# Optimization experiments

Hardware: AMD Instinct MI355X
Metric: run time of the kernel (lower is better)

Reference implementation:

```python
import math
import jax
import jax.numpy as jnp
import numpy as np

N_FFT = 2048
HOP = 512
WIN = 2048
N_FREQ = N_FFT // 2 + 1


def _make_buffers():
    # ISTFT synthesis kernel: inverse DFT basis with one-sided spectrum weights.
    n = np.arange(N_FFT, dtype=np.float32)
    k = np.arange(N_FREQ, dtype=np.float32)
    angles = 2.0 * np.pi * k[:, None] * n[None, :] / N_FFT
    w = np.full(N_FREQ, 2.0 / N_FFT, dtype=np.float32)
    w[0] = 1.0 / N_FFT
    if N_FFT % 2 == 0:
        w[-1] = 1.0 / N_FFT
    real_k = np.cos(angles) * w[:, None]
    imag_k = -np.sin(angles) * w[:, None]
    kernel = np.concatenate([real_k, imag_k], axis=0).astype(np.float32)  # [2*N_FREQ, N_FFT]
    # periodic Hann window (torch.hann_window default), win_length == n_fft so no pad
    win = (0.5 * (1.0 - np.cos(2.0 * np.pi * np.arange(WIN) / WIN))).astype(np.float32)
    window_sq = (win * win).astype(np.float32)
    return jnp.asarray(kernel), jnp.asarray(window_sq)


def setup_inputs() -> dict:
    key = jax.random.key(0)
    B, frames = 8, 2048
    stft_repr = jax.random.normal(key, (B, N_FREQ, frames, 2), dtype=jnp.float32)
    kernel, window_sq = _make_buffers()
    orig_len = (frames - 1) * HOP  # 1048064
    return {"stft_repr": stft_repr, "kernel": kernel, "window_sq": window_sq, "orig_len": orig_len}


def reference(stft_repr, kernel, window_sq, orig_len):
    B, n_freq, frames, _ = stft_repr.shape
    # stack real/imag channels: [B, 2*n_freq, frames]
    x = jnp.concatenate([stft_repr[..., 0], stft_repr[..., 1]], axis=1)
    # conv_transpose1d(stride=HOP) == per-frame synthesis GEMM + overlap-add
    contrib = jnp.einsum('bct,cn->btn', x, kernel)  # [B, frames, N_FFT]
    L = (frames - 1) * HOP + N_FFT
    idx = (jnp.arange(frames) * HOP)[:, None] + jnp.arange(N_FFT)[None, :]  # [frames, N_FFT]
    flat = idx.reshape(-1)
    audio = jnp.zeros((B, L), dtype=contrib.dtype).at[:, flat].add(contrib.reshape(B, -1))
    # normalization envelope: every frame fits (e <= L always, since L = (T-1)*hop + n_fft)
    env = jnp.zeros((L,), dtype=window_sq.dtype).at[flat].add(
        jnp.broadcast_to(window_sq, (frames, N_FFT)).reshape(-1))
    env = jnp.maximum(env, 1e-8)
    audio = audio / env[None, :]
    pad = N_FFT // 2
    return audio[:, pad:pad + orig_len]
```

## Files before the change

kernel.cpp:

```cpp
#include <hip/hip_runtime.h>
#include <math.h>

#define NFREQ 1025
#define NT 2048
#define NB 8
#define ORIG_LEN 1048064
#define FR 16
#define SEGS 13
#define NBLK 158
#define CROW 1026
#define PI_F 3.14159265358979323846f

__device__ __forceinline__ int cphys(int m) {
    return m ^ ((((m >> 5) ^ (m >> 8)) & 7) << 2);
}
__device__ __forceinline__ int tphys(int r) { return r + (r >> 4); }

__device__ __forceinline__ float2 cmul(float2 a, float2 b) {
    return make_float2(a.x * b.x - a.y * b.y, a.x * b.y + a.y * b.x);
}

template <int LEN, int TSTEP>
__device__ __forceinline__ void r4stage(float2* __restrict__ W,
                                        const float2* __restrict__ TW, int lane) {
#pragma unroll
    for (int c = 0; c < 4; ++c) {
        const int i = lane + (c << 6);
        const int quarter = LEN >> 2;
        const int grp = i / quarter, pos = i - grp * quarter;
        const int i0 = grp * LEN + pos;
        const int ia = cphys(i0), ib = cphys(i0 + quarter);
        const int ic = cphys(i0 + 2 * quarter), id = cphys(i0 + 3 * quarter);
        const float2 a = W[ia], bv = W[ib], cv = W[ic], dv = W[id];
        const float2 w1 = TW[tphys(pos * TSTEP)];
        const float2 w2 = cmul(w1, w1);
        const float2 w3 = cmul(w2, w1);
        const float2 t1 = cmul(bv, w1);
        const float2 t2 = cmul(cv, w2);
        const float2 t3 = cmul(dv, w3);
        W[ia] = make_float2(a.x + t1.x + t2.x + t3.x, a.y + t1.y + t2.y + t3.y);
        W[ib] = make_float2(a.x - t1.y - t2.x + t3.y, a.y + t1.x - t2.y - t3.x);
        W[ic] = make_float2(a.x - t1.x + t2.x - t3.x, a.y - t1.y + t2.y - t3.y);
        W[id] = make_float2(a.x + t1.y - t2.x - t3.y, a.y - t1.x - t2.y + t3.x);
    }
}

__global__ __launch_bounds__(1024) void istft_fused(const float* __restrict__ in,
                                                    float* __restrict__ out) {
    __shared__ float2 D[FR * CROW];
    __shared__ float2 TW[544];
    const int tid = threadIdx.x;
    const int lane = tid & 63, wv = tid >> 6;
    const int g = blockIdx.x, b = blockIdx.y;
    const int f0 = (g == 0) ? 0 : (13 * g - 1);
    const int sbase = 2 + 13 * g;
    const int nseg = (2049 - sbase < SEGS) ? (2049 - sbase) : SEGS;

    if (tid < 512) {
        float s, c;
        sincosf(6.28318530717958647692f * (float)tid * (1.0f / 1024.0f), &s, &c);
        TW[tphys(tid)] = make_float2(c, s);
    }

    const float* bbase = in + (size_t)b * NFREQ * (NT * 2);
#pragma unroll
    for (int it = 0; it < 17; ++it) {
        const int idx = tid + (it << 10);
        if (idx < FR * NFREQ) {
            const int k = idx >> 4, jf = idx & 15, ft = f0 + jf;
            float2 v2 = make_float2(0.0f, 0.0f);
            if (ft < NT) v2 = *(const float2*)(bbase + ((size_t)k * NT + ft) * 2);
            D[jf * CROW + k] = v2;
        }
    }
    __syncthreads();

    float2* W = D + wv * CROW;

    float2 v[16];
#pragma unroll
    for (int m = 0; m < 16; ++m) {
        const int jc = lane + (m << 6);
        const float2 xa = W[jc];
        const float2 xb = W[1024 - jc];
        const float Xr = xa.x, Xi = (jc == 0) ? 0.0f : xa.y;
        const float Cr = xb.x, Ci = (jc == 0) ? 0.0f : -xb.y;
        const float ar = Xr + Cr, ai = Xi + Ci;
        const float dr = Xr - Cr, di = Xi - Ci;
        float2 w = TW[tphys(jc >> 1)];
        if (jc & 1)
            w = cmul(w, make_float2(0.99999529380957617f, 0.00306795676296598f));
        const float br = dr * w.x - di * w.y;
        const float bi = dr * w.y + di * w.x;
        v[m] = make_float2((ar - bi) * (1.0f / 2048.0f), (ai + br) * (1.0f / 2048.0f));
    }
#pragma unroll
    for (int m0 = 0; m0 < 4; ++m0) {
        const float2 v0 = v[m0], v1 = v[m0 + 4], v2 = v[m0 + 8], v3 = v[m0 + 12];
        const int jb = lane + (m0 << 6);
        const int g8 = ((jb & 3) << 6) | (((jb >> 2) & 3) << 4) |
                       (((jb >> 4) & 3) << 2) | ((jb >> 6) & 3);
        const int p4 = cphys(g8 << 2);
        *(float4*)&W[p4]     = make_float4(v0.x + v1.x + v2.x + v3.x,
                                           v0.y + v1.y + v2.y + v3.y,
                                           v0.x - v1.y - v2.x + v3.y,
                                           v0.y + v1.x - v2.y - v3.x);
        *(float4*)&W[p4 + 2] = make_float4(v0.x - v1.x + v2.x - v3.x,
                                           v0.y - v1.y + v2.y - v3.y,
                                           v0.x + v1.y - v2.x - v3.y,
                                           v0.y - v1.x - v2.y + v3.x);
    }
    r4stage<16, 64>(W, TW, lane);
    r4stage<64, 16>(W, TW, lane);
    r4stage<256, 4>(W, TW, lane);
    r4stage<1024, 1>(W, TW, lane);
    __syncthreads();

    const int npairs = nseg << 8;
    float2* outb = (float2*)(out + (size_t)b * ORIG_LEN + (size_t)(sbase - 2) * 512);
#pragma unroll
    for (int it = 0; it < 4; ++it) {
        const int pj = tid + (it << 10);
        if (pj < npairs) {
            const int seg = pj >> 8, r2 = pj & 255;
            const int s = sbase + seg;
            const int qlo = (s == 2048) ? 1 : 0;
            const int qhi = (s == 2) ? 2 : 3;
            const int rowoff = (s - f0) * CROW;
            float ax = 0.0f, ay = 0.0f;
#pragma unroll
            for (int q = 0; q < 4; ++q) {
                if (q >= qlo && q <= qhi) {
                    const float2 c2 = D[rowoff - q * CROW + cphys((q << 8) + r2)];
                    ax += c2.x; ay += c2.y;
                }
            }
            float envx = 1.5f, envy = 1.5f;
            if (s == 2) {
                const int n0 = 1536 + (r2 << 1);
                const float wa = 0.5f - 0.5f * cosf((float)n0 * (PI_F / 1024.0f));
                const float wb = 0.5f - 0.5f * cosf((float)(n0 + 1) * (PI_F / 1024.0f));
                envx -= wa * wa; envy -= wb * wb;
            }
            if (s == 2048) {
                const int n0 = r2 << 1;
                const float wa = 0.5f - 0.5f * cosf((float)n0 * (PI_F / 1024.0f));
                const float wb = 0.5f - 0.5f * cosf((float)(n0 + 1) * (PI_F / 1024.0f));
                envx -= wa * wa; envy -= wb * wb;
            }
            outb[pj] = make_float2(ax / envx, ay / envy);
        }
    }
}

extern "C" void kernel_launch(void* const* d_in, const int* in_sizes, int n_in,
                              void* d_out, int out_size, void* d_ws, size_t ws_size,
                              hipStream_t stream) {
    const float* stft = (const float*)d_in[0];
    float* out = (float*)d_out;
    dim3 grid(NBLK, NB);
    istft_fused<<<grid, 1024, 0, stream>>>(stft, out);
}
```

Before: 291.6 us.

## Halve frames per block, remap blocks across XCDs, batch loads into registers

Blocks now handle 8 frames with 512 threads instead of 16 frames with 1024, so LDS per block shrinks and more blocks can be resident, at the cost of more recomputed overlap frames (3 halo frames per 5 output segments). The Nyquist bin is read directly from global into a register so each LDS row can drop to 1024 entries. Global loads are all issued into registers before any LDS stores to raise memory-level parallelism. Block indices are remapped so contiguous groups of blocks land on the same XCD for L2 locality. The larger halo fraction increases redundant FFT work and input reads.

```diff
diff --git a/kernel.cpp b/kernel.cpp
--- a/kernel.cpp
+++ b/kernel.cpp
@@ -5,10 +5,10 @@
 #define NT 2048
 #define NB 8
 #define ORIG_LEN 1048064
-#define FR 16
-#define SEGS 13
-#define NBLK 158
-#define CROW 1026
+#define FR 8
+#define SEGS 5
+#define NBLK 410
+#define CROW 1024
 #define PI_F 3.14159265358979323846f
 
 __device__ __forceinline__ int cphys(int m) {
@@ -45,15 +45,21 @@
     }
 }
 
-__global__ __launch_bounds__(1024) void istft_fused(const float* __restrict__ in,
-                                                    float* __restrict__ out) {
+__global__ __launch_bounds__(512) void istft_fused(const float* __restrict__ in,
+                                                   float* __restrict__ out) {
     __shared__ float2 D[FR * CROW];
     __shared__ float2 TW[544];
     const int tid = threadIdx.x;
     const int lane = tid & 63, wv = tid >> 6;
-    const int g = blockIdx.x, b = blockIdx.y;
-    const int f0 = (g == 0) ? 0 : (13 * g - 1);
-    const int sbase = 2 + 13 * g;
+
+    const unsigned bid = blockIdx.x;
+    const unsigned xcd = bid & 7u, jj = bid >> 3;
+    const unsigned qq = NBLK >> 3, rr = NBLK & 7u;
+    const int g = (int)((xcd < rr ? xcd * (qq + 1) : rr * (qq + 1) + (xcd - rr) * qq) + jj);
+    const int b = blockIdx.y;
+
+    const int f0 = (g == 0) ? 0 : (SEGS * g - 1);
+    const int sbase = 2 + SEGS * g;
     const int nseg = (2049 - sbase < SEGS) ? (2049 - sbase) : SEGS;
 
     if (tid < 512) {
@@ -63,15 +69,27 @@
     }
 
     const float* bbase = in + (size_t)b * NFREQ * (NT * 2);
+
+    float nyq = 0.0f;
+    {
+        const int ftw = f0 + wv;
+        if (lane == 0 && ftw < NT)
+            nyq = bbase[((size_t)1024 * NT + ftw) * 2];
+    }
+
+    float2 regs[16];
 #pragma unroll
-    for (int it = 0; it < 17; ++it) {
-        const int idx = tid + (it << 10);
-        if (idx < FR * NFREQ) {
-            const int k = idx >> 4, jf = idx & 15, ft = f0 + jf;
-            float2 v2 = make_float2(0.0f, 0.0f);
-            if (ft < NT) v2 = *(const float2*)(bbase + ((size_t)k * NT + ft) * 2);
-            D[jf * CROW + k] = v2;
-        }
+    for (int it = 0; it < 16; ++it) {
+        const int idx = tid + (it << 9);
+        const int k = idx >> 3, jf = idx & 7, ft = f0 + jf;
+        regs[it] = (ft < NT) ? *(const float2*)(bbase + ((size_t)k * NT + ft) * 2)
+                             : make_float2(0.0f, 0.0f);
+    }
+#pragma unroll
+    for (int it = 0; it < 16; ++it) {
+        const int idx = tid + (it << 9);
+        const int k = idx >> 3, jf = idx & 7;
+        D[jf * CROW + k] = regs[it];
     }
     __syncthreads();
 
@@ -82,7 +100,7 @@
     for (int m = 0; m < 16; ++m) {
         const int jc = lane + (m << 6);
         const float2 xa = W[jc];
-        const float2 xb = W[1024 - jc];
+        const float2 xb = (jc == 0) ? make_float2(nyq, 0.0f) : W[1024 - jc];
         const float Xr = xa.x, Xi = (jc == 0) ? 0.0f : xa.y;
         const float Cr = xb.x, Ci = (jc == 0) ? 0.0f : -xb.y;
         const float ar = Xr + Cr, ai = Xi + Ci;
@@ -119,8 +137,8 @@
     const int npairs = nseg << 8;
     float2* outb = (float2*)(out + (size_t)b * ORIG_LEN + (size_t)(sbase - 2) * 512);
 #pragma unroll
-    for (int it = 0; it < 4; ++it) {
-        const int pj = tid + (it << 10);
+    for (int it = 0; it < 3; ++it) {
+        const int pj = tid + (it << 9);
         if (pj < npairs) {
             const int seg = pj >> 8, r2 = pj & 255;
             const int s = sbase + seg;
@@ -159,5 +177,5 @@
     const float* stft = (const float*)d_in[0];
     float* out = (float*)d_out;
     dim3 grid(NBLK, NB);
-    istft_fused<<<grid, 1024, 0, stream>>>(stft, out);
+    istft_fused<<<grid, 512, 0, stream>>>(stft, out);
 }
```

New measurement: 257.0 us. 1.13x faster.
